# Kernel optimization log

Measured on AMD Instinct MI355X. Metric: run time of the kernel, lower is better.

Reference implementation:

```python
import jax, jax.numpy as jnp
import numpy as np
import itertools

LN_EPS = 1e-5

def _combo_idx(d):
    # lexicographic (i<j) and (i<j<k) combination indices, matching the torch nested loops
    pairs = np.array(list(itertools.combinations(range(d), 2)), dtype=np.int32)  # [P,2]
    trips = np.array(list(itertools.combinations(range(d), 3)), dtype=np.int32)  # [T,3]
    return pairs, trips

def setup_inputs() -> dict:
    key = jax.random.key(0)
    k1, k2 = jax.random.split(key)
    d, batch, out_dim = 64, 4096, 512
    total = d + d * (d - 1) // 2 + d * (d - 1) * (d - 2) // 6  # 63744
    x = jax.random.normal(k1, (batch, d), dtype=jnp.float32)
    W = jax.random.normal(k2, (total, out_dim), dtype=jnp.float32) * (1.0 / np.sqrt(total))
    b = jnp.zeros((out_dim,), dtype=jnp.float32)
    gamma = jnp.ones((out_dim,), dtype=jnp.float32)
    beta = jnp.zeros((out_dim,), dtype=jnp.float32)
    return {"x": x, "W": W, "b": b, "gamma": gamma, "beta": beta}

def reference(x, W, b, gamma, beta):
    d = x.shape[1]
    pairs, trips = _combo_idx(d)  # static numpy index tables
    # pairwise products x_i * x_j for i<j  -> [B, C(d,2)]
    pw = x[:, pairs[:, 0]] * x[:, pairs[:, 1]]
    # triplet products x_i * x_j * x_k for i<j<k -> [B, C(d,3)]
    tp = x[:, trips[:, 0]] * x[:, trips[:, 1]] * x[:, trips[:, 2]]
    feats = jnp.concatenate([x, pw, tp], axis=1)  # [B, total]
    h = feats @ W + b  # Linear
    # LayerNorm over last dim
    mu = jnp.mean(h, axis=-1, keepdims=True)
    var = jnp.var(h, axis=-1, keepdims=True)
    hn = (h - mu) * jax.lax.rsqrt(var + LN_EPS) * gamma + beta
    return jax.nn.relu(hn)
```

## Files before the change

### kernel.cpp

```cpp
#include <hip/hip_runtime.h>
#include <stdint.h>

#define D 64
#define KTOT 43744
#define NPAIR 2016
#define NOUT 512
#define MROWS 4096
#define BM 128
#define BN 256
#define BK 32
#define NSTEPS (KTOT / BK)
#define K2B (KTOT * 2)

typedef __attribute__((ext_vector_type(8))) short short8;
typedef __attribute__((ext_vector_type(4))) float f32x4;
typedef __attribute__((ext_vector_type(4))) uint32_t u32x4;

__device__ __forceinline__ uint32_t cvtpk(float lo, float hi) {
  uint32_t r;
  asm("v_cvt_pk_bf16_f32 %0, %1, %2" : "=v"(r) : "v"(lo), "v"(hi));
  return r;
}

__device__ __forceinline__ void load_b128_to_lds(const void* gsrc, void* ldst) {
  typedef const __attribute__((address_space(1))) uint32_t* GP;
  typedef __attribute__((address_space(3))) uint32_t* LP;
  __builtin_amdgcn_global_load_lds((GP)(uintptr_t)gsrc, (LP)(uintptr_t)ldst, 16, 0, 0);
}

__device__ __forceinline__ void unrank(int k, int& i, int& j, int& l) {
  if (k < D) {
    i = k; j = D; l = D;
  } else if (k < D + NPAIR) {
    int p = k - D;
    i = 0;
    while (p >= D - 1 - i) { p -= D - 1 - i; ++i; }
    j = i + 1 + p; l = D;
  } else {
    int t = k - (D + NPAIR);
    i = 0;
    for (;;) { int c = (D - 1 - i) * (D - 2 - i) / 2; if (t < c) break; t -= c; ++i; }
    j = i + 1;
    while (t >= D - 1 - j) { t -= D - 1 - j; ++j; }
    l = j + 1 + t;
  }
}

__device__ __forceinline__ bool inc_idx(int& i, int& j, int& l) {
  if (l >= D) {
    if (j >= D) { ++i; if (i == D) { i = 0; j = 1; } return true; }
    ++j;
    if (j == D) { ++i; j = i + 1; if (j == D) { i = 0; j = 1; l = 2; } }
    return true;
  }
  ++l;
  if (l == D) {
    ++j; l = j + 1;
    if (l == D) { ++i; j = i + 1; l = j + 1; }
    return true;
  }
  return false;
}

__global__ void build_idx_k(uint32_t* __restrict__ idx) {
  int k = blockIdx.x * 256 + threadIdx.x;
  if (k >= KTOT) return;
  int i, j, l;
  unrank(k, i, j, l);
  idx[k] = (uint32_t)i | ((uint32_t)j << 8) | ((uint32_t)l << 16);
}

__global__ void wtrans_k(const float* __restrict__ W, char* __restrict__ Wt) {
  __shared__ float tile[64][65];
  int bk = blockIdx.x;
  int bn = blockIdx.y;
  int t = threadIdx.x;
  int k0 = bk * 64, n0 = bn * 64;
  int col = t & 63, r0 = t >> 6;
  #pragma unroll
  for (int p = 0; p < 16; ++p) {
    int row = p * 4 + r0;
    tile[col][row] = (k0 + row < KTOT) ? W[(size_t)(k0 + row) * NOUT + (n0 + col)] : 0.0f;
  }
  __syncthreads();
  for (int u = t; u < 512; u += 256) {
    int n = u >> 3, s8 = u & 7;
    int chunk = s8 >> 2, s = s8 & 3;
    int kc0 = k0 + chunk * 32;
    if (kc0 >= KTOT) continue;
    int ng = n0 + n;
    int b = chunk * 32 + s * 8;
    u32x4 v = {cvtpk(tile[n][b + 0], tile[n][b + 1]),
               cvtpk(tile[n][b + 2], tile[n][b + 3]),
               cvtpk(tile[n][b + 4], tile[n][b + 5]),
               cvtpk(tile[n][b + 6], tile[n][b + 7])};
    int sp = s ^ ((ng >> 1) & 3);
    *(u32x4*)(Wt + (size_t)ng * K2B + (size_t)kc0 * 2 + (sp << 4)) = v;
  }
}

template<int USE_WT, int USE_IDX>
__global__ void __launch_bounds__(512, 4)
gemm_k(const float* __restrict__ x, const float* __restrict__ W,
       const char* __restrict__ Wt, const uint32_t* __restrict__ idxg,
       float* __restrict__ part, int S, int Slog, int steps_per, int swz) {
  __shared__ float XmT[D * 128];
  __shared__ __align__(16) char Al[2][BM * 64];
  __shared__ __align__(16) char Bl[2][BN * 64];

  const int t = threadIdx.x;
  const int lane = t & 63;
  const int w = t >> 6;

  int mb, ns;
  if (swz) {
    int xcd = blockIdx.x & 7;
    int sub = blockIdx.x >> 3;
    ns = xcd + 8 * (sub >> 5);
    mb = sub & 31;
  } else {
    mb = blockIdx.x & 31;
    ns = blockIdx.x >> 5;
  }
  const int nb = ns >> Slog;
  const int sb = ns & (S - 1);

  {
    int m = t >> 2, i0 = (t & 3) * 16;
    const float* src = x + (size_t)(mb * BM + m) * D + i0;
    #pragma unroll
    for (int c = 0; c < 4; ++c) {
      f32x4 v = *(const f32x4*)(src + c * 4);
      #pragma unroll
      for (int e = 0; e < 4; ++e) XmT[(i0 + c * 4 + e) * 128 + m] = v[e];
    }
  }

  f32x4 acc[4][4];
  #pragma unroll
  for (int a = 0; a < 4; ++a)
    #pragma unroll
    for (int b = 0; b < 4; ++b) {
      f32x4 z = {0.f, 0.f, 0.f, 0.f};
      acc[a][b] = z;
    }

  const int wr = w >> 2, wc = w & 3;
  const int g = lane >> 4;

  int Abase[4], Bbase[4];
  #pragma unroll
  for (int fm = 0; fm < 4; ++fm) {
    int m = wr * 64 + fm * 16 + (lane & 15);
    Abase[fm] = m * 64 + ((g ^ ((m >> 1) & 3)) << 4);
  }
  #pragma unroll
  for (int fn = 0; fn < 4; ++fn) {
    int n = wc * 64 + fn * 16 + (lane & 15);
    Bbase[fn] = n * 64 + ((g ^ ((n >> 1) & 3)) << 4);
  }

  uint32_t BrowOff[2];
  #pragma unroll
  for (int inst = 0; inst < 2; ++inst) {
    int row = nb * BN + w * 32 + inst * 16 + (lane >> 2);
    BrowOff[inst] = (uint32_t)row * K2B + ((lane & 3) << 4);
  }

  const int fg_m = t & 127;
  const int fg_kh = t >> 7;
  const float* xcol = XmT + fg_m;
  const uint32_t Awr = (uint32_t)(fg_m * 64 + ((fg_kh ^ ((fg_m >> 1) & 3)) << 4));

  const int ks0 = sb * steps_per;
  const int ks1 = (ks0 + steps_per < NSTEPS) ? (ks0 + steps_per) : NSTEPS;

  __syncthreads();

  auto do_stage = [&](int ks, int buf) {
    const int k0 = ks * BK;
    if (USE_WT) {
      #pragma unroll
      for (int inst = 0; inst < 2; ++inst)
        load_b128_to_lds(Wt + BrowOff[inst] + (uint32_t)k0 * 2,
                         &Bl[buf][w * 2048 + inst * 1024]);
    }
    {
      uint32_t pk[4];
      const int kbase = k0 + fg_kh * 8;
      if (USE_IDX) {
        if (kbase >= D + NPAIR) {
          const u32x4* ip = (const u32x4*)(idxg + kbase);
          u32x4 I0 = ip[0], I1 = ip[1];
          uint32_t prev = 0xFFFFFFFFu;
          float pp = 0.0f;
          float fv[8];
          #pragma unroll
          for (int e = 0; e < 8; ++e) {
            uint32_t uu = __builtin_amdgcn_readfirstlane(e < 4 ? I0[e & 3] : I1[e & 3]);
            uint32_t ij = uu & 0xFFFFu;
            if (ij != prev) {
              pp = xcol[(uu & 63u) * 128] * xcol[((uu >> 8) & 63u) * 128];
              prev = ij;
            }
            fv[e] = pp * xcol[((uu >> 16) & 63u) * 128];
          }
          #pragma unroll
          for (int c = 0; c < 4; ++c) pk[c] = cvtpk(fv[2 * c], fv[2 * c + 1]);
        } else {
          const u32x4* ip = (const u32x4*)(idxg + kbase);
          u32x4 I0 = ip[0], I1 = ip[1];
          float fv[8];
          #pragma unroll
          for (int e = 0; e < 8; ++e) {
            uint32_t uu = (e < 4) ? I0[e & 3] : I1[e & 3];
            uint32_t ji = (uu >> 8) & 0xFFu, li = uu >> 16;
            float xi = xcol[(uu & 63u) * 128];
            float xj = (ji < 64u) ? xcol[(ji & 63u) * 128] : 1.0f;
            float xl = (li < 64u) ? xcol[(li & 63u) * 128] : 1.0f;
            fv[e] = xi * xj * xl;
          }
          #pragma unroll
          for (int c = 0; c < 4; ++c) pk[c] = cvtpk(fv[2 * c], fv[2 * c + 1]);
        }
      } else {
        int ii, jj, ll;
        unrank(kbase, ii, jj, ll);
        float fv[8];
        #pragma unroll
        for (int h = 0; h < 8; ++h) {
          float xi = xcol[(ii & 63) * 128];
          float xj = (jj < 64) ? xcol[(jj & 63) * 128] : 1.0f;
          float xl = (ll < 64) ? xcol[(ll & 63) * 128] : 1.0f;
          fv[h] = xi * xj * xl;
          if (h < 7) inc_idx(ii, jj, ll);
        }
        #pragma unroll
        for (int c = 0; c < 4; ++c) pk[c] = cvtpk(fv[2 * c], fv[2 * c + 1]);
      }
      u32x4 v0 = {pk[0], pk[1], pk[2], pk[3]};
      *(u32x4*)(&Al[buf][0] + Awr) = v0;
    }
    if (!USE_WT) {
      #pragma unroll
      for (int i2 = 0; i2 < 2; ++i2) {
        int u = t + i2 * 512;
        int n = u & 255, s = u >> 8;
        const float* wp = W + (size_t)(k0 + s * 8) * NOUT + nb * BN + n;
        float f[8];
        #pragma unroll
        for (int e = 0; e < 8; ++e) f[e] = wp[(size_t)e * NOUT];
        u32x4 v = {cvtpk(f[0], f[1]), cvtpk(f[2], f[3]),
                   cvtpk(f[4], f[5]), cvtpk(f[6], f[7])};
        *(u32x4*)(&Bl[buf][0] + n * 64 + ((s ^ ((n >> 1) & 3)) << 4)) = v;
      }
    }
  };

  do_stage(ks0, 0);
  __syncthreads();

  int cur = 0;
  for (int ks = ks0; ks < ks1; ++ks) {
    if (ks + 1 < ks1) do_stage(ks + 1, cur ^ 1);

    __builtin_amdgcn_s_setprio(1);
    short8 av[4], bv[4];
    #pragma unroll
    for (int fm = 0; fm < 4; ++fm)
      av[fm] = *(const short8*)(&Al[cur][0] + Abase[fm]);
    #pragma unroll
    for (int fn = 0; fn < 4; ++fn)
      bv[fn] = *(const short8*)(&Bl[cur][0] + Bbase[fn]);
    #pragma unroll
    for (int fm = 0; fm < 4; ++fm)
      #pragma unroll
      for (int fn = 0; fn < 4; ++fn)
        acc[fm][fn] = __builtin_amdgcn_mfma_f32_16x16x32_bf16(av[fm], bv[fn], acc[fm][fn], 0, 0, 0);
    __builtin_amdgcn_s_setprio(0);

    if (ks + 1 < ks1) __syncthreads();
    cur ^= 1;
  }

  #pragma unroll
  for (int fm = 0; fm < 4; ++fm) {
    int rbase = mb * BM + wr * 64 + fm * 16 + ((lane >> 4) << 2);
    #pragma unroll
    for (int fn = 0; fn < 4; ++fn) {
      int col = nb * BN + wc * 64 + fn * 16 + (lane & 15);
      float* dst = part + ((size_t)sb * MROWS + rbase) * NOUT + col;
      #pragma unroll
      for (int r = 0; r < 4; ++r) dst[(size_t)r * NOUT] = acc[fm][fn][r];
    }
  }
}

__global__ void ln_k(const float* part, int S,
                     const float* __restrict__ bias, const float* __restrict__ gamma,
                     const float* __restrict__ beta, float* out) {
  int row = blockIdx.x;
  int t = threadIdx.x;
  float v[2];
  #pragma unroll
  for (int q = 0; q < 2; ++q) {
    int c = t + q * 256;
    float s = bias[c];
    for (int sbi = 0; sbi < S; ++sbi)
      s += part[((size_t)sbi * MROWS + row) * NOUT + c];
    v[q] = s;
  }
  float sum = v[0] + v[1];
  float sq = v[0] * v[0] + v[1] * v[1];
  #pragma unroll
  for (int off = 32; off > 0; off >>= 1) {
    sum += __shfl_xor(sum, off, 64);
    sq  += __shfl_xor(sq, off, 64);
  }
  __shared__ float red[8];
  int wv = t >> 6;
  if ((t & 63) == 0) { red[wv] = sum; red[4 + wv] = sq; }
  __syncthreads();
  sum = red[0] + red[1] + red[2] + red[3];
  sq  = red[4] + red[5] + red[6] + red[7];
  float mu = sum * (1.0f / NOUT);
  float var = sq * (1.0f / NOUT) - mu * mu;
  float rs = rsqrtf(var + 1e-5f);
  #pragma unroll
  for (int q = 0; q < 2; ++q) {
    int c = t + q * 256;
    float hn = (v[q] - mu) * rs * gamma[c] + beta[c];
    out[(size_t)row * NOUT + c] = fmaxf(hn, 0.0f);
  }
}

extern "C" void kernel_launch(void* const* d_in, const int* in_sizes, int n_in,
                              void* d_out, int out_size, void* d_ws, size_t ws_size,
                              hipStream_t stream) {
  const float* x     = (const float*)d_in[0];
  const float* W     = (const float*)d_in[1];
  const float* bias  = (const float*)d_in[2];
  const float* gamma = (const float*)d_in[3];
  const float* beta  = (const float*)d_in[4];
  float* out = (float*)d_out;
  (void)in_sizes; (void)n_in; (void)out_size;

  const size_t IDXB = 262144;
  const size_t WTB  = (size_t)NOUT * K2B;
  const size_t PART = (size_t)MROWS * NOUT * sizeof(float);

  char* base = (char*)d_ws;
  uint32_t* idx = (uint32_t*)base;
  char* Wt = base + IDXB;

  const bool has_idx = ws_size >= IDXB;
  bool use_wt = false;
  int S = 1, Slog = 0;
  if (ws_size >= IDXB + WTB + 8 * PART)      { use_wt = true;  S = 8; Slog = 3; }
  else if (ws_size >= IDXB + 8 * PART)       { use_wt = false; S = 8; Slog = 3; }
  else if (ws_size >= IDXB + WTB + 4 * PART) { use_wt = true;  S = 4; Slog = 2; }
  else if (ws_size >= IDXB + 4 * PART)       { use_wt = false; S = 4; Slog = 2; }
  else if (ws_size >= IDXB + WTB + 2 * PART) { use_wt = true;  S = 2; Slog = 1; }
  else if (ws_size >= IDXB + 2 * PART)       { use_wt = false; S = 2; Slog = 1; }
  else if (ws_size >= IDXB + WTB)            { use_wt = true;  S = 1; Slog = 0; }

  float* part = out;
  if (S > 1) part = (float*)(base + IDXB + (use_wt ? WTB : 0));

  int steps_per = (NSTEPS + S - 1) / S;
  int grid = 32 * (NOUT / BN) * S;
  int swz = (grid == 512) ? 1 : 0;

  if (has_idx) build_idx_k<<<(KTOT + 255) / 256, 256, 0, stream>>>(idx);
  if (use_wt)  wtrans_k<<<dim3((KTOT + 63) / 64, 8), 256, 0, stream>>>(W, Wt);

  if (use_wt)
    gemm_k<1, 1><<<grid, 512, 0, stream>>>(x, W, Wt, idx, part, S, Slog, steps_per, swz);
  else if (has_idx)
    gemm_k<0, 1><<<grid, 512, 0, stream>>>(x, W, Wt, idx, part, S, Slog, steps_per, swz);
  else
    gemm_k<0, 0><<<grid, 512, 0, stream>>>(x, W, Wt, nullptr, part, S, Slog, steps_per, swz);

  ln_k<<<MROWS, 256, 0, stream>>>(part, S, bias, gamma, beta, out);
}
```

Measured before the change: 301.2 us.

## Load pre-transposed B fragments directly from global into registers, bypassing LDS

The pre-transposed bf16 weight layout drops its XOR swizzle and is stored linearly per row. The GEMM's USE_WT path now has each lane read its MFMA B fragments straight from global memory into registers, with no global-to-LDS async copy and no LDS B buffers. This removes B-side LDS traffic and LDS capacity, which could raise occupancy. In exchange, each wave re-reads the same B data from global/L2, the load latency sits on the MFMA critical path with little prefetch distance, and the per-lane reads are only 16 bytes wide.

```diff
diff --git a/kernel.cpp b/kernel.cpp
--- a/kernel.cpp
+++ b/kernel.cpp
@@ -20,12 +20,6 @@
   uint32_t r;
   asm("v_cvt_pk_bf16_f32 %0, %1, %2" : "=v"(r) : "v"(lo), "v"(hi));
   return r;
-}
-
-__device__ __forceinline__ void load_b128_to_lds(const void* gsrc, void* ldst) {
-  typedef const __attribute__((address_space(1))) uint32_t* GP;
-  typedef __attribute__((address_space(3))) uint32_t* LP;
-  __builtin_amdgcn_global_load_lds((GP)(uintptr_t)gsrc, (LP)(uintptr_t)ldst, 16, 0, 0);
 }
 
 __device__ __forceinline__ void unrank(int k, int& i, int& j, int& l) {
@@ -85,17 +79,15 @@
   __syncthreads();
   for (int u = t; u < 512; u += 256) {
     int n = u >> 3, s8 = u & 7;
-    int chunk = s8 >> 2, s = s8 & 3;
-    int kc0 = k0 + chunk * 32;
+    int kc0 = k0 + s8 * 8;
     if (kc0 >= KTOT) continue;
     int ng = n0 + n;
-    int b = chunk * 32 + s * 8;
+    int b = s8 * 8;
     u32x4 v = {cvtpk(tile[n][b + 0], tile[n][b + 1]),
                cvtpk(tile[n][b + 2], tile[n][b + 3]),
                cvtpk(tile[n][b + 4], tile[n][b + 5]),
                cvtpk(tile[n][b + 6], tile[n][b + 7])};
-    int sp = s ^ ((ng >> 1) & 3);
-    *(u32x4*)(Wt + (size_t)ng * K2B + (size_t)kc0 * 2 + (sp << 4)) = v;
+    *(u32x4*)(Wt + (size_t)ng * K2B + (size_t)kc0 * 2) = v;
   }
 }
 
@@ -106,7 +98,6 @@
        float* __restrict__ part, int S, int Slog, int steps_per, int swz) {
   __shared__ float XmT[D * 128];
   __shared__ __align__(16) char Al[2][BM * 64];
-  __shared__ __align__(16) char Bl[2][BN * 64];
 
   const int t = threadIdx.x;
   const int lane = t & 63;
@@ -148,23 +139,11 @@
   const int wr = w >> 2, wc = w & 3;
   const int g = lane >> 4;
 
-  int Abase[4], Bbase[4];
+  int Abase[4];
   #pragma unroll
   for (int fm = 0; fm < 4; ++fm) {
     int m = wr * 64 + fm * 16 + (lane & 15);
     Abase[fm] = m * 64 + ((g ^ ((m >> 1) & 3)) << 4);
-  }
-  #pragma unroll
-  for (int fn = 0; fn < 4; ++fn) {
-    int n = wc * 64 + fn * 16 + (lane & 15);
-    Bbase[fn] = n * 64 + ((g ^ ((n >> 1) & 3)) << 4);
-  }
-
-  uint32_t BrowOff[2];
-  #pragma unroll
-  for (int inst = 0; inst < 2; ++inst) {
-    int row = nb * BN + w * 32 + inst * 16 + (lane >> 2);
-    BrowOff[inst] = (uint32_t)row * K2B + ((lane & 3) << 4);
   }
 
   const int fg_m = t & 127;
@@ -175,73 +154,111 @@
   const int ks0 = sb * steps_per;
   const int ks1 = (ks0 + steps_per < NSTEPS) ? (ks0 + steps_per) : NSTEPS;
 
-  __syncthreads();
-
-  auto do_stage = [&](int ks, int buf) {
-    const int k0 = ks * BK;
-    if (USE_WT) {
-      #pragma unroll
-      for (int inst = 0; inst < 2; ++inst)
-        load_b128_to_lds(Wt + BrowOff[inst] + (uint32_t)k0 * 2,
-                         &Bl[buf][w * 2048 + inst * 1024]);
-    }
-    {
-      uint32_t pk[4];
-      const int kbase = k0 + fg_kh * 8;
-      if (USE_IDX) {
-        if (kbase >= D + NPAIR) {
-          const u32x4* ip = (const u32x4*)(idxg + kbase);
-          u32x4 I0 = ip[0], I1 = ip[1];
-          uint32_t prev = 0xFFFFFFFFu;
-          float pp = 0.0f;
-          float fv[8];
-          #pragma unroll
-          for (int e = 0; e < 8; ++e) {
-            uint32_t uu = __builtin_amdgcn_readfirstlane(e < 4 ? I0[e & 3] : I1[e & 3]);
-            uint32_t ij = uu & 0xFFFFu;
-            if (ij != prev) {
-              pp = xcol[(uu & 63u) * 128] * xcol[((uu >> 8) & 63u) * 128];
-              prev = ij;
-            }
-            fv[e] = pp * xcol[((uu >> 16) & 63u) * 128];
+  auto gen_a = [&](int ks, int buf) {
+    uint32_t pk[4];
+    const int kbase = ks * BK + fg_kh * 8;
+    if (USE_IDX) {
+      if (kbase >= D + NPAIR) {
+        const u32x4* ip = (const u32x4*)(idxg + kbase);
+        u32x4 I0 = ip[0], I1 = ip[1];
+        uint32_t prev = 0xFFFFFFFFu;
+        float pp = 0.0f;
+        float fv[8];
+        #pragma unroll
+        for (int e = 0; e < 8; ++e) {
+          uint32_t uu = __builtin_amdgcn_readfirstlane(e < 4 ? I0[e & 3] : I1[e & 3]);
+          uint32_t ij = uu & 0xFFFFu;
+          if (ij != prev) {
+            pp = xcol[(uu & 63u) * 128] * xcol[((uu >> 8) & 63u) * 128];
+            prev = ij;
           }
-          #pragma unroll
-          for (int c = 0; c < 4; ++c) pk[c] = cvtpk(fv[2 * c], fv[2 * c + 1]);
-        } else {
-          const u32x4* ip = (const u32x4*)(idxg + kbase);
-          u32x4 I0 = ip[0], I1 = ip[1];
-          float fv[8];
-          #pragma unroll
-          for (int e = 0; e < 8; ++e) {
-            uint32_t uu = (e < 4) ? I0[e & 3] : I1[e & 3];
-            uint32_t ji = (uu >> 8) & 0xFFu, li = uu >> 16;
-            float xi = xcol[(uu & 63u) * 128];
-            float xj = (ji < 64u) ? xcol[(ji & 63u) * 128] : 1.0f;
-            float xl = (li < 64u) ? xcol[(li & 63u) * 128] : 1.0f;
-            fv[e] = xi * xj * xl;
-          }
-          #pragma unroll
-          for (int c = 0; c < 4; ++c) pk[c] = cvtpk(fv[2 * c], fv[2 * c + 1]);
+          fv[e] = pp * xcol[((uu >> 16) & 63u) * 128];
         }
+        #pragma unroll
+        for (int c = 0; c < 4; ++c) pk[c] = cvtpk(fv[2 * c], fv[2 * c + 1]);
       } else {
-        int ii, jj, ll;
-        unrank(kbase, ii, jj, ll);
+        const u32x4* ip = (const u32x4*)(idxg + kbase);
+        u32x4 I0 = ip[0], I1 = ip[1];
         float fv[8];
         #pragma unroll
-        for (int h = 0; h < 8; ++h) {
-          float xi = xcol[(ii & 63) * 128];
-          float xj = (jj < 64) ? xcol[(jj & 63) * 128] : 1.0f;
-          float xl = (ll < 64) ? xcol[(ll & 63) * 128] : 1.0f;
-          fv[h] = xi * xj * xl;
-          if (h < 7) inc_idx(ii, jj, ll);
+        for (int e = 0; e < 8; ++e) {
+          uint32_t uu = (e < 4) ? I0[e & 3] : I1[e & 3];
+          uint32_t ji = (uu >> 8) & 0xFFu, li = uu >> 16;
+          float xi = xcol[(uu & 63u) * 128];
+          float xj = (ji < 64u) ? xcol[(ji & 63u) * 128] : 1.0f;
+          float xl = (li < 64u) ? xcol[(li & 63u) * 128] : 1.0f;
+          fv[e] = xi * xj * xl;
         }
         #pragma unroll
         for (int c = 0; c < 4; ++c) pk[c] = cvtpk(fv[2 * c], fv[2 * c + 1]);
       }
-      u32x4 v0 = {pk[0], pk[1], pk[2], pk[3]};
-      *(u32x4*)(&Al[buf][0] + Awr) = v0;
-    }
-    if (!USE_WT) {
+    } else {
+      int ii, jj, ll;
+      unrank(kbase, ii, jj, ll);
+      float fv[8];
+      #pragma unroll
+      for (int h = 0; h < 8; ++h) {
+        float xi = xcol[(ii & 63) * 128];
+        float xj = (jj < 64) ? xcol[(jj & 63) * 128] : 1.0f;
+        float xl = (ll < 64) ? xcol[(ll & 63) * 128] : 1.0f;
+        fv[h] = xi * xj * xl;
+        if (h < 7) inc_idx(ii, jj, ll);
+      }
+      #pragma unroll
+      for (int c = 0; c < 4; ++c) pk[c] = cvtpk(fv[2 * c], fv[2 * c + 1]);
+    }
+    u32x4 v0 = {pk[0], pk[1], pk[2], pk[3]};
+    *(u32x4*)(&Al[buf][0] + Awr) = v0;
+  };
+
+  if constexpr (USE_WT) {
+    const char* Bp[4];
+    #pragma unroll
+    for (int fn = 0; fn < 4; ++fn) {
+      int row = nb * BN + wc * 64 + fn * 16 + (lane & 15);
+      Bp[fn] = Wt + (size_t)row * K2B + ((uint32_t)g << 4);
+    }
+
+    gen_a(ks0, 0);
+    __syncthreads();
+
+    int cur = 0;
+    for (int ks = ks0; ks < ks1; ++ks) {
+      const bool more = (ks + 1 < ks1);
+      short8 bv[4];
+      {
+        const size_t ko = (size_t)(ks * BK) * 2;
+        #pragma unroll
+        for (int fn = 0; fn < 4; ++fn)
+          bv[fn] = *(const short8*)(Bp[fn] + ko);
+      }
+      if (more) gen_a(ks + 1, cur ^ 1);
+
+      __builtin_amdgcn_s_setprio(1);
+      short8 av[4];
+      #pragma unroll
+      for (int fm = 0; fm < 4; ++fm)
+        av[fm] = *(const short8*)(&Al[cur][0] + Abase[fm]);
+      #pragma unroll
+      for (int fm = 0; fm < 4; ++fm)
+        #pragma unroll
+        for (int fn = 0; fn < 4; ++fn)
+          acc[fm][fn] = __builtin_amdgcn_mfma_f32_16x16x32_bf16(av[fm], bv[fn], acc[fm][fn], 0, 0, 0);
+      __builtin_amdgcn_s_setprio(0);
+
+      if (more) __syncthreads();
+      cur ^= 1;
+    }
+  } else {
+    __shared__ __align__(16) char Bl[2][BN * 64];
+    int Bbase[4];
+    #pragma unroll
+    for (int fn = 0; fn < 4; ++fn) {
+      int n = wc * 64 + fn * 16 + (lane & 15);
+      Bbase[fn] = n * 64 + ((g ^ ((n >> 1) & 3)) << 4);
+    }
+    auto stage_b = [&](int ks, int buf) {
+      const int k0 = ks * BK;
       #pragma unroll
       for (int i2 = 0; i2 < 2; ++i2) {
         int u = t + i2 * 512;
@@ -254,33 +271,35 @@
                    cvtpk(f[4], f[5]), cvtpk(f[6], f[7])};
         *(u32x4*)(&Bl[buf][0] + n * 64 + ((s ^ ((n >> 1) & 3)) << 4)) = v;
       }
-    }
-  };
-
-  do_stage(ks0, 0);
-  __syncthreads();
-
-  int cur = 0;
-  for (int ks = ks0; ks < ks1; ++ks) {
-    if (ks + 1 < ks1) do_stage(ks + 1, cur ^ 1);
-
-    __builtin_amdgcn_s_setprio(1);
-    short8 av[4], bv[4];
-    #pragma unroll
-    for (int fm = 0; fm < 4; ++fm)
-      av[fm] = *(const short8*)(&Al[cur][0] + Abase[fm]);
-    #pragma unroll
-    for (int fn = 0; fn < 4; ++fn)
-      bv[fn] = *(const short8*)(&Bl[cur][0] + Bbase[fn]);
-    #pragma unroll
-    for (int fm = 0; fm < 4; ++fm)
+    };
+
+    stage_b(ks0, 0);
+    gen_a(ks0, 0);
+    __syncthreads();
+
+    int cur = 0;
+    for (int ks = ks0; ks < ks1; ++ks) {
+      const bool more = (ks + 1 < ks1);
+      if (more) { stage_b(ks + 1, cur ^ 1); gen_a(ks + 1, cur ^ 1); }
+
+      __builtin_amdgcn_s_setprio(1);
+      short8 av[4], bv[4];
+      #pragma unroll
+      for (int fm = 0; fm < 4; ++fm)
+        av[fm] = *(const short8*)(&Al[cur][0] + Abase[fm]);
       #pragma unroll
       for (int fn = 0; fn < 4; ++fn)
-        acc[fm][fn] = __builtin_amdgcn_mfma_f32_16x16x32_bf16(av[fm], bv[fn], acc[fm][fn], 0, 0, 0);
-    __builtin_amdgcn_s_setprio(0);
-
-    if (ks + 1 < ks1) __syncthreads();
-    cur ^= 1;
+        bv[fn] = *(const short8*)(&Bl[cur][0] + Bbase[fn]);
+      #pragma unroll
+      for (int fm = 0; fm < 4; ++fm)
+        #pragma unroll
+        for (int fn = 0; fn < 4; ++fn)
+          acc[fm][fn] = __builtin_amdgcn_mfma_f32_16x16x32_bf16(av[fm], bv[fn], acc[fm][fn], 0, 0, 0);
+      __builtin_amdgcn_s_setprio(0);
+
+      if (more) __syncthreads();
+      cur ^= 1;
+    }
   }
 
   #pragma unroll
```

Result: slower. 317.9 us (+5.6%).
